# Performance work log

Measured on AMD Instinct MI355X. Metric: run time of the kernel, lower is better.

The kernel has to match this reference:

```python
import jax, jax.numpy as jnp
import numpy as np

N = 10000        # nodes
E = 640000       # edges (before self-loops)
IN = 128         # in_channels
HID = 32         # hidden_channels
HEADS = 4
HC = HID * HEADS # 128
OUT = 40         # out_channels
NEG_SLOPE = 0.2  # PyG GATConv default


def setup_inputs() -> dict:
    key = jax.random.key(0)
    ks = jax.random.split(key, 12)
    g = lambda k, shape: (jax.random.normal(k, shape, jnp.float32) * 0.1)
    return {
        "x": jax.random.normal(ks[0], (N, IN), jnp.float32),
        "edge_index": jax.random.randint(ks[1], (2, E), 0, N, dtype=jnp.int32),
        # conv1: in -> HID per head, HEADS heads, concat
        "W1": g(ks[2], (IN, HEADS * HID)),
        "a_src1": g(ks[3], (HEADS, HID)),
        "a_dst1": g(ks[4], (HEADS, HID)),
        "b1": jnp.zeros((HEADS * HID,), jnp.float32),
        # conv2: HC -> HC, 1 head
        "W2": g(ks[5], (HC, HC)),
        "a_src2": g(ks[6], (1, HC)),
        "a_dst2": g(ks[7], (1, HC)),
        "b2": jnp.zeros((HC,), jnp.float32),
        # final linear head
        "Wlin": g(ks[8], (HC, OUT)),
        "blin": jnp.zeros((OUT,), jnp.float32),
    }


def _gat_layer(x, W, a_src, a_dst, b, src, dst, heads, n):
    """PyG-style GATConv: gather -> edge attention -> segment softmax -> scatter."""
    d = W.shape[1] // heads
    h = (x @ W).reshape(n, heads, d)                       # [N, H, d]
    asrc = jnp.einsum('nhd,hd->nh', h, a_src)              # [N, H]
    adst = jnp.einsum('nhd,hd->nh', h, a_dst)
    e = jax.nn.leaky_relu(asrc[src] + adst[dst], NEG_SLOPE)  # [E, H]
    m = jax.ops.segment_max(e, dst, num_segments=n)          # per-dst max (stable softmax)
    p = jnp.exp(e - m[dst])
    z = jax.ops.segment_sum(p, dst, num_segments=n)
    alpha = p / (z[dst] + 1e-16)                             # [E, H]
    out = jax.ops.segment_sum(h[src] * alpha[:, :, None], dst, num_segments=n)
    return out.reshape(n, heads * d) + b


def reference(x, edge_index, W1, a_src1, a_dst1, b1, W2, a_src2, a_dst2, b2, Wlin, blin):
    n = x.shape[0]
    loop = jnp.arange(n, dtype=edge_index.dtype)           # add_self_loops=True
    src = jnp.concatenate([edge_index[0], loop])
    dst = jnp.concatenate([edge_index[1], loop])
    # eval mode: dropout is identity
    h1 = jax.nn.elu(_gat_layer(x, W1, a_src1, a_dst1, b1, src, dst, HEADS, n))
    h2 = jax.nn.elu(_gat_layer(h1, W2, a_src2, a_dst2, b2, src, dst, 1, n))
    return h2 @ Wlin + blin
```

## Files before the change

### kernel.cpp

```cpp
#include <hip/hip_runtime.h>
#include <hip/hip_bf16.h>

#define CAP 192

__global__ void fused_csr_gemm4(const int* __restrict__ srcArr, const int* __restrict__ dstArr,
                                int E, int N, int* __restrict__ deg, int* __restrict__ csr,
                                const float* __restrict__ x, const float* __restrict__ W,
                                const float* __restrict__ a_src, const float* __restrict__ a_dst,
                                __hip_bfloat16* __restrict__ hwb, float* __restrict__ asrc,
                                float* __restrict__ adst, int NC) {
    __shared__ float xr[8][128];
    int tid = threadIdx.x;
    if ((int)blockIdx.x < NC) {
        int Etot = E + N;
        int base = blockIdx.x * 512 + tid;
#pragma unroll
        for (int k = 0; k < 4; k++) {
            int i = base + k * 128;
            if (i < Etot) {
                int s, d;
                if (i < E) { s = srcArr[i]; d = dstArr[i]; }
                else       { s = d = i - E; }
                int p = atomicAdd(&deg[d], 1);
                if (p < CAP) csr[d * CAP + p] = s;
            }
        }
        return;
    }
    const int NB = 8;
    int n0 = (blockIdx.x - NC) * NB;
    int j = tid;
    for (int r = 0; r < NB; r++) {
        int nn = n0 + r;
        xr[r][j] = (nn < N) ? x[nn * 128 + j] : 0.f;
    }
    __syncthreads();
    float acc[NB];
#pragma unroll
    for (int r = 0; r < NB; r++) acc[r] = 0.f;
    for (int k = 0; k < 128; k++) {
        float w = W[k * 128 + j];
#pragma unroll
        for (int r = 0; r < NB; r++) acc[r] += xr[r][k] * w;
    }
    int h = j >> 5;
    float as = a_src[j];
    float ad = a_dst[j];
    for (int r = 0; r < NB; r++) {
        int nn = n0 + r;
        if (nn < N) hwb[nn * 128 + j] = __float2bfloat16(acc[r]);
        float vs = acc[r] * as;
        float vd = acc[r] * ad;
        for (int off = 16; off >= 1; off >>= 1) {
            vs += __shfl_xor(vs, off);
            vd += __shfl_xor(vd, off);
        }
        if ((j & 31) == 0 && nn < N) { asrc[nn * 4 + h] = vs; adst[nn * 4 + h] = vd; }
    }
}

__global__ void gemm_att1(const float* __restrict__ x, const float* __restrict__ W,
                          const float* __restrict__ a_src, const float* __restrict__ a_dst,
                          __hip_bfloat16* __restrict__ hwb, float* __restrict__ asrc,
                          float* __restrict__ adst, int N) {
    const int NB = 8;
    int n0 = blockIdx.x * NB;
    int j = threadIdx.x;
    __shared__ float xr[NB][128];
    __shared__ float tmp[4];
    for (int r = 0; r < NB; r++) {
        int nn = n0 + r;
        xr[r][j] = (nn < N) ? x[nn * 128 + j] : 0.f;
    }
    __syncthreads();
    float acc[NB];
#pragma unroll
    for (int r = 0; r < NB; r++) acc[r] = 0.f;
    for (int k = 0; k < 128; k++) {
        float w = W[k * 128 + j];
#pragma unroll
        for (int r = 0; r < NB; r++) acc[r] += xr[r][k] * w;
    }
    float as = a_src[j];
    float ad = a_dst[j];
    for (int r = 0; r < NB; r++) {
        int nn = n0 + r;
        if (nn < N) hwb[nn * 128 + j] = __float2bfloat16(acc[r]);
        float vs = acc[r] * as;
        float vd = acc[r] * ad;
        for (int off = 32; off >= 1; off >>= 1) {
            vs += __shfl_xor(vs, off);
            vd += __shfl_xor(vd, off);
        }
        if ((j & 63) == 0) { tmp[(j >> 6) * 2] = vs; tmp[(j >> 6) * 2 + 1] = vd; }
        __syncthreads();
        if (j == 0 && nn < N) { asrc[nn] = tmp[0] + tmp[2]; adst[nn] = tmp[1] + tmp[3]; }
        __syncthreads();
    }
}

__global__ void agg4(const __hip_bfloat16* __restrict__ hw, const float* __restrict__ asrc,
                     const float* __restrict__ adst, const int* __restrict__ degArr,
                     const int* __restrict__ csr_src, const float* __restrict__ b,
                     float* __restrict__ y, int N) {
    const int H = 4;
    int n = blockIdx.x;
    int t = threadIdx.x;
    int g = t >> 5;
    int lane = t & 31;
    int beg = n * CAP;
    int deg = min(degArr[n], CAP);
    const unsigned short* hwu = (const unsigned short*)hw;
    __shared__ float pe[128 * H];
    __shared__ int se[128];
    __shared__ float adl[H];
    __shared__ float red[4 * 128];
    __shared__ float zred[2 * H];
    if (t < H) adl[t] = adst[n * H + t];
    int hcol = lane >> 3;
    float4 acc = make_float4(0.f, 0.f, 0.f, 0.f);
    float zp[H];
#pragma unroll
    for (int hh = 0; hh < H; hh++) zp[hh] = 0.f;
    for (int base = 0; base < deg; base += 128) {
        int cnt = min(128, deg - base);
        __syncthreads();
        if (t < cnt) {
            int s = csr_src[beg + base + t];
            se[t] = s;
            float4 av = *(const float4*)&asrc[s * 4];
            float e0 = av.x + adl[0], e1 = av.y + adl[1];
            float e2 = av.z + adl[2], e3 = av.w + adl[3];
            e0 = e0 > 0.f ? e0 : 0.2f * e0;
            e1 = e1 > 0.f ? e1 : 0.2f * e1;
            e2 = e2 > 0.f ? e2 : 0.2f * e2;
            e3 = e3 > 0.f ? e3 : 0.2f * e3;
            float p0 = __expf(e0), p1 = __expf(e1), p2 = __expf(e2), p3 = __expf(e3);
            pe[t * 4 + 0] = p0; pe[t * 4 + 1] = p1;
            pe[t * 4 + 2] = p2; pe[t * 4 + 3] = p3;
            zp[0] += p0; zp[1] += p1; zp[2] += p2; zp[3] += p3;
        }
        __syncthreads();
        for (int c = g; c < cnt; c += 4) {
            int s = se[c];
            float p = pe[c * 4 + hcol];
            uint2 v = *(const uint2*)&hwu[s * 128 + lane * 4];
            float f0 = __uint_as_float(v.x << 16);
            float f1 = __uint_as_float(v.x & 0xffff0000u);
            float f2 = __uint_as_float(v.y << 16);
            float f3 = __uint_as_float(v.y & 0xffff0000u);
            acc.x += p * f0; acc.y += p * f1; acc.z += p * f2; acc.w += p * f3;
        }
    }
    ((float4*)&red[g * 128])[lane] = acc;
#pragma unroll
    for (int hh = 0; hh < H; hh++) {
        float v = zp[hh];
        for (int off = 32; off >= 1; off >>= 1) v += __shfl_xor(v, off);
        if ((t & 63) == 0) zred[(t >> 6) * H + hh] = v;
    }
    __syncthreads();
    float total = red[t] + red[128 + t] + red[256 + t] + red[384 + t];
    int h = t >> 5;
    float z = zred[h] + zred[H + h];
    float res = total / (z + 1e-16f) + b[t];
    y[n * 128 + t] = res > 0.f ? res : (__expf(res) - 1.0f);
}

__global__ void agg1_lin(const __hip_bfloat16* __restrict__ hw, const float* __restrict__ asrc,
                         const float* __restrict__ adst, const int* __restrict__ degArr,
                         const int* __restrict__ csr_src, const float* __restrict__ b,
                         const float* __restrict__ Wl, const float* __restrict__ bl,
                         float* __restrict__ out, int N, int OUTC) {
    int n = blockIdx.x;
    int t = threadIdx.x;
    int g = t >> 5;
    int lane = t & 31;
    int beg = n * CAP;
    int deg = min(degArr[n], CAP);
    const unsigned short* hwu = (const unsigned short*)hw;
    __shared__ float pe[128];
    __shared__ int se[128];
    __shared__ float adl;
    __shared__ float red[4 * 128];
    __shared__ float zred[2];
    __shared__ float yrow[128];
    if (t == 0) adl = adst[n];
    float4 acc = make_float4(0.f, 0.f, 0.f, 0.f);
    float zp = 0.f;
    for (int base = 0; base < deg; base += 128) {
        int cnt = min(128, deg - base);
        __syncthreads();
        if (t < cnt) {
            int s = csr_src[beg + base + t];
            se[t] = s;
            float e = asrc[s] + adl;
            e = e > 0.f ? e : 0.2f * e;
            float p = __expf(e);
            pe[t] = p;
            zp += p;
        }
        __syncthreads();
        for (int c = g; c < cnt; c += 4) {
            int s = se[c];
            float p = pe[c];
            uint2 v = *(const uint2*)&hwu[s * 128 + lane * 4];
            float f0 = __uint_as_float(v.x << 16);
            float f1 = __uint_as_float(v.x & 0xffff0000u);
            float f2 = __uint_as_float(v.y << 16);
            float f3 = __uint_as_float(v.y & 0xffff0000u);
            acc.x += p * f0; acc.y += p * f1; acc.z += p * f2; acc.w += p * f3;
        }
    }
    ((float4*)&red[g * 128])[lane] = acc;
    {
        float v = zp;
        for (int off = 32; off >= 1; off >>= 1) v += __shfl_xor(v, off);
        if ((t & 63) == 0) zred[t >> 6] = v;
    }
    __syncthreads();
    float total = red[t] + red[128 + t] + red[256 + t] + red[384 + t];
    float z = zred[0] + zred[1];
    float res = total / (z + 1e-16f) + b[t];
    yrow[t] = res > 0.f ? res : (__expf(res) - 1.0f);
    __syncthreads();
    if (t < OUTC) {
        float a = bl[t];
        for (int k = 0; k < 128; k++) a += yrow[k] * Wl[k * OUTC + t];
        out[n * OUTC + t] = a;
    }
}

extern "C" void kernel_launch(void* const* d_in, const int* in_sizes, int n_in,
                              void* d_out, int out_size, void* d_ws, size_t ws_size,
                              hipStream_t stream) {
    const float* x       = (const float*)d_in[0];
    const int*   ei      = (const int*)d_in[1];
    const float* W1      = (const float*)d_in[2];
    const float* a_src1  = (const float*)d_in[3];
    const float* a_dst1  = (const float*)d_in[4];
    const float* b1      = (const float*)d_in[5];
    const float* W2      = (const float*)d_in[6];
    const float* a_src2  = (const float*)d_in[7];
    const float* a_dst2  = (const float*)d_in[8];
    const float* b2      = (const float*)d_in[9];
    const float* Wlin    = (const float*)d_in[10];
    const float* blin    = (const float*)d_in[11];
    float* out = (float*)d_out;

    const int N = in_sizes[0] / 128;
    const int E = in_sizes[1] / 2;
    const int OUTC = in_sizes[10] / 128;
    const int Etot = E + N;
    const int* src = ei;
    const int* dst = ei + E;
    const int NG = (N + 7) / 8;
    const int NC = (Etot + 511) / 512;

    char* w = (char*)d_ws;
    size_t off = 0;
    auto alloc = [&](size_t bytes) -> char* {
        char* p = w + off;
        off += (bytes + 255) & ~(size_t)255;
        return p;
    };
    int*             deg   = (int*)alloc((size_t)N * 4);
    int*             csr   = (int*)alloc((size_t)N * CAP * 4);
    __hip_bfloat16*  hwb   = (__hip_bfloat16*)alloc((size_t)N * 128 * 2);
    float*           bufY  = (float*)alloc((size_t)N * 128 * 4);
    float*           asrc1 = (float*)alloc((size_t)N * 4 * 4);
    float*           adst1 = (float*)alloc((size_t)N * 4 * 4);
    float*           asrc2 = (float*)alloc((size_t)N * 4);
    float*           adst2 = (float*)alloc((size_t)N * 4);
    (void)ws_size;

    hipMemsetAsync(deg, 0, (size_t)N * 4, stream);
    fused_csr_gemm4<<<NC + NG, 128, 0, stream>>>(src, dst, E, N, deg, csr,
                                                 x, W1, a_src1, a_dst1, hwb, asrc1, adst1, NC);

    agg4<<<N, 128, 0, stream>>>(hwb, asrc1, adst1, deg, csr, b1, bufY, N);

    gemm_att1<<<NG, 128, 0, stream>>>(bufY, W2, a_src2, a_dst2, hwb, asrc2, adst2, N);
    agg1_lin<<<N, 128, 0, stream>>>(hwb, asrc2, adst2, deg, csr, b2, Wlin, blin, out, N, OUTC);
}
```

Before: 204.4 us.

## Split per-node degree counters into four sub-buckets and interleave CSR/GEMM blocks

```diff
diff --git a/kernel.cpp b/kernel.cpp
--- a/kernel.cpp
+++ b/kernel.cpp
@@ -2,18 +2,23 @@
 #include <hip/hip_bf16.h>
 
 #define CAP 192
+#define SUBCAP 48
 
 __global__ void fused_csr_gemm4(const int* __restrict__ srcArr, const int* __restrict__ dstArr,
-                                int E, int N, int* __restrict__ deg, int* __restrict__ csr,
+                                int E, int N, int* __restrict__ deg2, int* __restrict__ csr,
                                 const float* __restrict__ x, const float* __restrict__ W,
                                 const float* __restrict__ a_src, const float* __restrict__ a_dst,
                                 __hip_bfloat16* __restrict__ hwb, float* __restrict__ asrc,
-                                float* __restrict__ adst, int NC) {
+                                float* __restrict__ adst, int NC, int NG) {
     __shared__ float xr[8][128];
     int tid = threadIdx.x;
-    if ((int)blockIdx.x < NC) {
+    int pair = blockIdx.x >> 1;
+    if ((blockIdx.x & 1) == 0) {
+        if (pair >= NC) return;
+        int k_sub = pair & 3;
+        int* degk = deg2 + k_sub * N;
         int Etot = E + N;
-        int base = blockIdx.x * 512 + tid;
+        int base = pair * 512 + tid;
 #pragma unroll
         for (int k = 0; k < 4; k++) {
             int i = base + k * 128;
@@ -21,14 +26,15 @@
                 int s, d;
                 if (i < E) { s = srcArr[i]; d = dstArr[i]; }
                 else       { s = d = i - E; }
-                int p = atomicAdd(&deg[d], 1);
-                if (p < CAP) csr[d * CAP + p] = s;
+                int p = atomicAdd(&degk[d], 1);
+                if (p < SUBCAP) csr[d * CAP + k_sub * SUBCAP + p] = s;
             }
         }
         return;
     }
+    if (pair >= NG) return;
     const int NB = 8;
-    int n0 = (blockIdx.x - NC) * NB;
+    int n0 = pair * NB;
     int j = tid;
     for (int r = 0; r < NB; r++) {
         int nn = n0 + r;
@@ -99,8 +105,17 @@
     }
 }
 
+__device__ __forceinline__ int seg_slot(int idx, int p1, int p2, int p3, int n) {
+    int k, off;
+    if (idx < p1)      { k = 0; off = idx; }
+    else if (idx < p2) { k = 1; off = idx - p1; }
+    else if (idx < p3) { k = 2; off = idx - p2; }
+    else               { k = 3; off = idx - p3; }
+    return n * CAP + k * SUBCAP + off;
+}
+
 __global__ void agg4(const __hip_bfloat16* __restrict__ hw, const float* __restrict__ asrc,
-                     const float* __restrict__ adst, const int* __restrict__ degArr,
+                     const float* __restrict__ adst, const int* __restrict__ deg2,
                      const int* __restrict__ csr_src, const float* __restrict__ b,
                      float* __restrict__ y, int N) {
     const int H = 4;
@@ -108,8 +123,12 @@
     int t = threadIdx.x;
     int g = t >> 5;
     int lane = t & 31;
-    int beg = n * CAP;
-    int deg = min(degArr[n], CAP);
+    int d0 = min(deg2[0 * N + n], SUBCAP);
+    int d1 = min(deg2[1 * N + n], SUBCAP);
+    int d2 = min(deg2[2 * N + n], SUBCAP);
+    int d3 = min(deg2[3 * N + n], SUBCAP);
+    int p1 = d0, p2 = d0 + d1, p3 = p2 + d2;
+    int deg = p3 + d3;
     const unsigned short* hwu = (const unsigned short*)hw;
     __shared__ float pe[128 * H];
     __shared__ int se[128];
@@ -126,7 +145,7 @@
         int cnt = min(128, deg - base);
         __syncthreads();
         if (t < cnt) {
-            int s = csr_src[beg + base + t];
+            int s = csr_src[seg_slot(base + t, p1, p2, p3, n)];
             se[t] = s;
             float4 av = *(const float4*)&asrc[s * 4];
             float e0 = av.x + adl[0], e1 = av.y + adl[1];
@@ -135,10 +154,10 @@
             e1 = e1 > 0.f ? e1 : 0.2f * e1;
             e2 = e2 > 0.f ? e2 : 0.2f * e2;
             e3 = e3 > 0.f ? e3 : 0.2f * e3;
-            float p0 = __expf(e0), p1 = __expf(e1), p2 = __expf(e2), p3 = __expf(e3);
-            pe[t * 4 + 0] = p0; pe[t * 4 + 1] = p1;
-            pe[t * 4 + 2] = p2; pe[t * 4 + 3] = p3;
-            zp[0] += p0; zp[1] += p1; zp[2] += p2; zp[3] += p3;
+            float p0 = __expf(e0), pp1 = __expf(e1), pp2 = __expf(e2), pp3 = __expf(e3);
+            pe[t * 4 + 0] = p0; pe[t * 4 + 1] = pp1;
+            pe[t * 4 + 2] = pp2; pe[t * 4 + 3] = pp3;
+            zp[0] += p0; zp[1] += pp1; zp[2] += pp2; zp[3] += pp3;
         }
         __syncthreads();
         for (int c = g; c < cnt; c += 4) {
@@ -168,7 +187,7 @@
 }
 
 __global__ void agg1_lin(const __hip_bfloat16* __restrict__ hw, const float* __restrict__ asrc,
-                         const float* __restrict__ adst, const int* __restrict__ degArr,
+                         const float* __restrict__ adst, const int* __restrict__ deg2,
                          const int* __restrict__ csr_src, const float* __restrict__ b,
                          const float* __restrict__ Wl, const float* __restrict__ bl,
                          float* __restrict__ out, int N, int OUTC) {
@@ -176,8 +195,12 @@
     int t = threadIdx.x;
     int g = t >> 5;
     int lane = t & 31;
-    int beg = n * CAP;
-    int deg = min(degArr[n], CAP);
+    int d0 = min(deg2[0 * N + n], SUBCAP);
+    int d1 = min(deg2[1 * N + n], SUBCAP);
+    int d2 = min(deg2[2 * N + n], SUBCAP);
+    int d3 = min(deg2[3 * N + n], SUBCAP);
+    int p1 = d0, p2 = d0 + d1, p3 = p2 + d2;
+    int deg = p3 + d3;
     const unsigned short* hwu = (const unsigned short*)hw;
     __shared__ float pe[128];
     __shared__ int se[128];
@@ -192,7 +215,7 @@
         int cnt = min(128, deg - base);
         __syncthreads();
         if (t < cnt) {
-            int s = csr_src[beg + base + t];
+            int s = csr_src[seg_slot(base + t, p1, p2, p3, n)];
             se[t] = s;
             float e = asrc[s] + adl;
             e = e > 0.f ? e : 0.2f * e;
@@ -256,6 +279,7 @@
     const int* dst = ei + E;
     const int NG = (N + 7) / 8;
     const int NC = (Etot + 511) / 512;
+    const int NMAX = (NC > NG) ? NC : NG;
 
     char* w = (char*)d_ws;
     size_t off = 0;
@@ -264,7 +288,7 @@
         off += (bytes + 255) & ~(size_t)255;
         return p;
     };
-    int*             deg   = (int*)alloc((size_t)N * 4);
+    int*             deg2  = (int*)alloc((size_t)4 * N * 4);
     int*             csr   = (int*)alloc((size_t)N * CAP * 4);
     __hip_bfloat16*  hwb   = (__hip_bfloat16*)alloc((size_t)N * 128 * 2);
     float*           bufY  = (float*)alloc((size_t)N * 128 * 4);
@@ -274,12 +298,13 @@
     float*           adst2 = (float*)alloc((size_t)N * 4);
     (void)ws_size;
 
-    hipMemsetAsync(deg, 0, (size_t)N * 4, stream);
-    fused_csr_gemm4<<<NC + NG, 128, 0, stream>>>(src, dst, E, N, deg, csr,
-                                                 x, W1, a_src1, a_dst1, hwb, asrc1, adst1, NC);
-
-    agg4<<<N, 128, 0, stream>>>(hwb, asrc1, adst1, deg, csr, b1, bufY, N);
+    hipMemsetAsync(deg2, 0, (size_t)4 * N * 4, stream);
+    fused_csr_gemm4<<<2 * NMAX, 128, 0, stream>>>(src, dst, E, N, deg2, csr,
+                                                  x, W1, a_src1, a_dst1, hwb, asrc1, adst1,
+                                                  NC, NG);
+
+    agg4<<<N, 128, 0, stream>>>(hwb, asrc1, adst1, deg2, csr, b1, bufY, N);
 
     gemm_att1<<<NG, 128, 0, stream>>>(bufY, W2, a_src2, a_dst2, hwb, asrc2, adst2, N);
-    agg1_lin<<<N, 128, 0, stream>>>(hwb, asrc2, adst2, deg, csr, b2, Wlin, blin, out, N, OUTC);
-}
+    agg1_lin<<<N, 128, 0, stream>>>(hwb, asrc2, adst2, deg2, csr, b2, Wlin, blin, out, N, OUTC);
+}
```

After: 183.6 us. 10.2% less time.

## Split CSR degree counters into sub-buckets and shrink aggregation blocks to one wavefront

Applied to the files above, without the earlier changes.

```diff
diff --git a/kernel.cpp b/kernel.cpp
--- a/kernel.cpp
+++ b/kernel.cpp
@@ -1,19 +1,24 @@
 #include <hip/hip_runtime.h>
 #include <hip/hip_bf16.h>
 
-#define CAP 192
+#define KSUB 8
+#define SUBCAP 32
+#define CAP 256
 
 __global__ void fused_csr_gemm4(const int* __restrict__ srcArr, const int* __restrict__ dstArr,
-                                int E, int N, int* __restrict__ deg, int* __restrict__ csr,
+                                int E, int N, int* __restrict__ deg2, int* __restrict__ csr,
                                 const float* __restrict__ x, const float* __restrict__ W,
                                 const float* __restrict__ a_src, const float* __restrict__ a_dst,
                                 __hip_bfloat16* __restrict__ hwb, float* __restrict__ asrc,
-                                float* __restrict__ adst, int NC) {
+                                float* __restrict__ adst, int NC, int NG) {
     __shared__ float xr[8][128];
     int tid = threadIdx.x;
-    if ((int)blockIdx.x < NC) {
+    int pair = blockIdx.x >> 1;
+    if ((blockIdx.x & 1) == 0) {
+        if (pair >= NC) return;
+        int k_sub = pair & (KSUB - 1);
         int Etot = E + N;
-        int base = blockIdx.x * 512 + tid;
+        int base = pair * 512 + tid;
 #pragma unroll
         for (int k = 0; k < 4; k++) {
             int i = base + k * 128;
@@ -21,14 +26,15 @@
                 int s, d;
                 if (i < E) { s = srcArr[i]; d = dstArr[i]; }
                 else       { s = d = i - E; }
-                int p = atomicAdd(&deg[d], 1);
-                if (p < CAP) csr[d * CAP + p] = s;
+                int p = atomicAdd(&deg2[d * KSUB + k_sub], 1);
+                if (p < SUBCAP) csr[d * CAP + k_sub * SUBCAP + p] = s;
             }
         }
         return;
     }
+    if (pair >= NG) return;
     const int NB = 8;
-    int n0 = (blockIdx.x - NC) * NB;
+    int n0 = pair * NB;
     int j = tid;
     for (int r = 0; r < NB; r++) {
         int nn = n0 + r;
@@ -99,38 +105,44 @@
     }
 }
 
-__global__ void agg4(const __hip_bfloat16* __restrict__ hw, const float* __restrict__ asrc,
-                     const float* __restrict__ adst, const int* __restrict__ degArr,
-                     const int* __restrict__ csr_src, const float* __restrict__ b,
-                     float* __restrict__ y, int N) {
-    const int H = 4;
+__device__ __forceinline__ int slot8(int idx, const int* pref) {
+    int k = 0;
+#pragma unroll
+    for (int j = 1; j < KSUB; j++) k += (idx >= pref[j]);
+    return k * SUBCAP + (idx - pref[k]);
+}
+
+__global__ __launch_bounds__(64) void agg4(const __hip_bfloat16* __restrict__ hw,
+                     const float* __restrict__ asrc, const float* __restrict__ adst,
+                     const int* __restrict__ deg2, const int* __restrict__ csr_src,
+                     const float* __restrict__ b, float* __restrict__ y, int N) {
     int n = blockIdx.x;
     int t = threadIdx.x;
-    int g = t >> 5;
-    int lane = t & 31;
-    int beg = n * CAP;
-    int deg = min(degArr[n], CAP);
-    const unsigned short* hwu = (const unsigned short*)hw;
-    __shared__ float pe[128 * H];
-    __shared__ int se[128];
-    __shared__ float adl[H];
-    __shared__ float red[4 * 128];
-    __shared__ float zred[2 * H];
-    if (t < H) adl[t] = adst[n * H + t];
-    int hcol = lane >> 3;
-    float4 acc = make_float4(0.f, 0.f, 0.f, 0.f);
-    float zp[H];
-#pragma unroll
-    for (int hh = 0; hh < H; hh++) zp[hh] = 0.f;
-    for (int base = 0; base < deg; base += 128) {
-        int cnt = min(128, deg - base);
+    const int4* dp = (const int4*)&deg2[n * KSUB];
+    int4 ca = dp[0], cb = dp[1];
+    int pref[KSUB];
+    int cnts[KSUB] = { min(ca.x,SUBCAP), min(ca.y,SUBCAP), min(ca.z,SUBCAP), min(ca.w,SUBCAP),
+                       min(cb.x,SUBCAP), min(cb.y,SUBCAP), min(cb.z,SUBCAP), min(cb.w,SUBCAP) };
+    pref[0] = 0;
+#pragma unroll
+    for (int k = 1; k < KSUB; k++) pref[k] = pref[k-1] + cnts[k-1];
+    int deg = pref[KSUB-1] + cnts[KSUB-1];
+    const unsigned* hwu = (const unsigned*)hw;
+    __shared__ float pe[64 * 4];
+    __shared__ int se[64];
+    float4 adl = *(const float4*)&adst[n * 4];
+    int hcol = t >> 4;
+    float2 acc = make_float2(0.f, 0.f);
+    float z0 = 0.f, z1 = 0.f, z2 = 0.f, z3 = 0.f;
+    for (int base = 0; base < deg; base += 64) {
+        int cnt = min(64, deg - base);
         __syncthreads();
         if (t < cnt) {
-            int s = csr_src[beg + base + t];
+            int s = csr_src[n * CAP + slot8(base + t, pref)];
             se[t] = s;
             float4 av = *(const float4*)&asrc[s * 4];
-            float e0 = av.x + adl[0], e1 = av.y + adl[1];
-            float e2 = av.z + adl[2], e3 = av.w + adl[3];
+            float e0 = av.x + adl.x, e1 = av.y + adl.y;
+            float e2 = av.z + adl.z, e3 = av.w + adl.w;
             e0 = e0 > 0.f ? e0 : 0.2f * e0;
             e1 = e1 > 0.f ? e1 : 0.2f * e1;
             e2 = e2 > 0.f ? e2 : 0.2f * e2;
@@ -138,61 +150,60 @@
             float p0 = __expf(e0), p1 = __expf(e1), p2 = __expf(e2), p3 = __expf(e3);
             pe[t * 4 + 0] = p0; pe[t * 4 + 1] = p1;
             pe[t * 4 + 2] = p2; pe[t * 4 + 3] = p3;
-            zp[0] += p0; zp[1] += p1; zp[2] += p2; zp[3] += p3;
-        }
-        __syncthreads();
-        for (int c = g; c < cnt; c += 4) {
+            z0 += p0; z1 += p1; z2 += p2; z3 += p3;
+        }
+        __syncthreads();
+        for (int c = 0; c < cnt; c++) {
             int s = se[c];
             float p = pe[c * 4 + hcol];
-            uint2 v = *(const uint2*)&hwu[s * 128 + lane * 4];
-            float f0 = __uint_as_float(v.x << 16);
-            float f1 = __uint_as_float(v.x & 0xffff0000u);
-            float f2 = __uint_as_float(v.y << 16);
-            float f3 = __uint_as_float(v.y & 0xffff0000u);
-            acc.x += p * f0; acc.y += p * f1; acc.z += p * f2; acc.w += p * f3;
-        }
-    }
-    ((float4*)&red[g * 128])[lane] = acc;
-#pragma unroll
-    for (int hh = 0; hh < H; hh++) {
-        float v = zp[hh];
-        for (int off = 32; off >= 1; off >>= 1) v += __shfl_xor(v, off);
-        if ((t & 63) == 0) zred[(t >> 6) * H + hh] = v;
-    }
-    __syncthreads();
-    float total = red[t] + red[128 + t] + red[256 + t] + red[384 + t];
-    int h = t >> 5;
-    float z = zred[h] + zred[H + h];
-    float res = total / (z + 1e-16f) + b[t];
-    y[n * 128 + t] = res > 0.f ? res : (__expf(res) - 1.0f);
-}
-
-__global__ void agg1_lin(const __hip_bfloat16* __restrict__ hw, const float* __restrict__ asrc,
-                         const float* __restrict__ adst, const int* __restrict__ degArr,
-                         const int* __restrict__ csr_src, const float* __restrict__ b,
-                         const float* __restrict__ Wl, const float* __restrict__ bl,
-                         float* __restrict__ out, int N, int OUTC) {
+            unsigned v = hwu[s * 64 + t];
+            acc.x += p * __uint_as_float(v << 16);
+            acc.y += p * __uint_as_float(v & 0xffff0000u);
+        }
+    }
+    for (int off = 32; off >= 1; off >>= 1) {
+        z0 += __shfl_xor(z0, off); z1 += __shfl_xor(z1, off);
+        z2 += __shfl_xor(z2, off); z3 += __shfl_xor(z3, off);
+    }
+    float z = (hcol == 0) ? z0 : (hcol == 1) ? z1 : (hcol == 2) ? z2 : z3;
+    float inv = 1.f / (z + 1e-16f);
+    float2 bb = *(const float2*)&b[t * 2];
+    float r0 = acc.x * inv + bb.x;
+    float r1 = acc.y * inv + bb.y;
+    r0 = r0 > 0.f ? r0 : (__expf(r0) - 1.0f);
+    r1 = r1 > 0.f ? r1 : (__expf(r1) - 1.0f);
+    *(float2*)&y[n * 128 + t * 2] = make_float2(r0, r1);
+}
+
+__global__ __launch_bounds__(64) void agg1_lin(const __hip_bfloat16* __restrict__ hw,
+                         const float* __restrict__ asrc, const float* __restrict__ adst,
+                         const int* __restrict__ deg2, const int* __restrict__ csr_src,
+                         const float* __restrict__ b, const float* __restrict__ Wl,
+                         const float* __restrict__ bl, float* __restrict__ out,
+                         int N, int OUTC) {
     int n = blockIdx.x;
     int t = threadIdx.x;
-    int g = t >> 5;
-    int lane = t & 31;
-    int beg = n * CAP;
-    int deg = min(degArr[n], CAP);
-    const unsigned short* hwu = (const unsigned short*)hw;
-    __shared__ float pe[128];
-    __shared__ int se[128];
-    __shared__ float adl;
-    __shared__ float red[4 * 128];
-    __shared__ float zred[2];
+    const int4* dp = (const int4*)&deg2[n * KSUB];
+    int4 ca = dp[0], cb = dp[1];
+    int pref[KSUB];
+    int cnts[KSUB] = { min(ca.x,SUBCAP), min(ca.y,SUBCAP), min(ca.z,SUBCAP), min(ca.w,SUBCAP),
+                       min(cb.x,SUBCAP), min(cb.y,SUBCAP), min(cb.z,SUBCAP), min(cb.w,SUBCAP) };
+    pref[0] = 0;
+#pragma unroll
+    for (int k = 1; k < KSUB; k++) pref[k] = pref[k-1] + cnts[k-1];
+    int deg = pref[KSUB-1] + cnts[KSUB-1];
+    const unsigned* hwu = (const unsigned*)hw;
+    __shared__ float pe[64];
+    __shared__ int se[64];
     __shared__ float yrow[128];
-    if (t == 0) adl = adst[n];
-    float4 acc = make_float4(0.f, 0.f, 0.f, 0.f);
+    float adl = adst[n];
+    float2 acc = make_float2(0.f, 0.f);
     float zp = 0.f;
-    for (int base = 0; base < deg; base += 128) {
-        int cnt = min(128, deg - base);
+    for (int base = 0; base < deg; base += 64) {
+        int cnt = min(64, deg - base);
         __syncthreads();
         if (t < cnt) {
-            int s = csr_src[beg + base + t];
+            int s = csr_src[n * CAP + slot8(base + t, pref)];
             se[t] = s;
             float e = asrc[s] + adl;
             e = e > 0.f ? e : 0.2f * e;
@@ -201,28 +212,22 @@
             zp += p;
         }
         __syncthreads();
-        for (int c = g; c < cnt; c += 4) {
+        for (int c = 0; c < cnt; c++) {
             int s = se[c];
             float p = pe[c];
-            uint2 v = *(const uint2*)&hwu[s * 128 + lane * 4];
-            float f0 = __uint_as_float(v.x << 16);
-            float f1 = __uint_as_float(v.x & 0xffff0000u);
-            float f2 = __uint_as_float(v.y << 16);
-            float f3 = __uint_as_float(v.y & 0xffff0000u);
-            acc.x += p * f0; acc.y += p * f1; acc.z += p * f2; acc.w += p * f3;
-        }
-    }
-    ((float4*)&red[g * 128])[lane] = acc;
-    {
-        float v = zp;
-        for (int off = 32; off >= 1; off >>= 1) v += __shfl_xor(v, off);
-        if ((t & 63) == 0) zred[t >> 6] = v;
-    }
-    __syncthreads();
-    float total = red[t] + red[128 + t] + red[256 + t] + red[384 + t];
-    float z = zred[0] + zred[1];
-    float res = total / (z + 1e-16f) + b[t];
-    yrow[t] = res > 0.f ? res : (__expf(res) - 1.0f);
+            unsigned v = hwu[s * 64 + t];
+            acc.x += p * __uint_as_float(v << 16);
+            acc.y += p * __uint_as_float(v & 0xffff0000u);
+        }
+    }
+    for (int off = 32; off >= 1; off >>= 1) zp += __shfl_xor(zp, off);
+    float inv = 1.f / (zp + 1e-16f);
+    float2 bb = *(const float2*)&b[t * 2];
+    float r0 = acc.x * inv + bb.x;
+    float r1 = acc.y * inv + bb.y;
+    r0 = r0 > 0.f ? r0 : (__expf(r0) - 1.0f);
+    r1 = r1 > 0.f ? r1 : (__expf(r1) - 1.0f);
+    yrow[t * 2] = r0; yrow[t * 2 + 1] = r1;
     __syncthreads();
     if (t < OUTC) {
         float a = bl[t];
@@ -256,6 +261,7 @@
     const int* dst = ei + E;
     const int NG = (N + 7) / 8;
     const int NC = (Etot + 511) / 512;
+    const int NMAX = (NC > NG) ? NC : NG;
 
     char* w = (char*)d_ws;
     size_t off = 0;
@@ -264,7 +270,7 @@
         off += (bytes + 255) & ~(size_t)255;
         return p;
     };
-    int*             deg   = (int*)alloc((size_t)N * 4);
+    int*             deg2  = (int*)alloc((size_t)N * KSUB * 4);
     int*             csr   = (int*)alloc((size_t)N * CAP * 4);
     __hip_bfloat16*  hwb   = (__hip_bfloat16*)alloc((size_t)N * 128 * 2);
     float*           bufY  = (float*)alloc((size_t)N * 128 * 4);
@@ -274,12 +280,13 @@
     float*           adst2 = (float*)alloc((size_t)N * 4);
     (void)ws_size;
 
-    hipMemsetAsync(deg, 0, (size_t)N * 4, stream);
-    fused_csr_gemm4<<<NC + NG, 128, 0, stream>>>(src, dst, E, N, deg, csr,
-                                                 x, W1, a_src1, a_dst1, hwb, asrc1, adst1, NC);
-
-    agg4<<<N, 128, 0, stream>>>(hwb, asrc1, adst1, deg, csr, b1, bufY, N);
+    hipMemsetAsync(deg2, 0, (size_t)N * KSUB * 4, stream);
+    fused_csr_gemm4<<<2 * NMAX, 128, 0, stream>>>(src, dst, E, N, deg2, csr,
+                                                  x, W1, a_src1, a_dst1, hwb, asrc1, adst1,
+                                                  NC, NG);
+
+    agg4<<<N, 64, 0, stream>>>(hwb, asrc1, adst1, deg2, csr, b1, bufY, N);
 
     gemm_att1<<<NG, 128, 0, stream>>>(bufY, W2, a_src2, a_dst2, hwb, asrc2, adst2, N);
-    agg1_lin<<<N, 128, 0, stream>>>(hwb, asrc2, adst2, deg, csr, b2, Wlin, blin, out, N, OUTC);
-}
+    agg1_lin<<<N, 64, 0, stream>>>(hwb, asrc2, adst2, deg2, csr, b2, Wlin, blin, out, N, OUTC);
+}
```

Result: faster. 174.6 us (-14.6%).
